# Kernel tuning notes

Hardware: AMD Instinct MI355X
Metric: run time of the kernel (lower is better)

The kernel has to match this reference:

```python
import jax, jax.numpy as jnp
import numpy as np

L, D, H, DH, DI, V, S, B = 12, 768, 12, 64, 3072, 32000, 512, 2
LN_EPS = 1e-3  # keras LayerNormalization default epsilon

def _gelu(x):
    return x * 0.5 * (1.0 + jnp.tanh(np.sqrt(2.0 / np.pi).astype(np.float32) * (x + 0.044715 * x ** 3)))

def _layer_norm(x, g, b):
    mu = jnp.mean(x, axis=-1, keepdims=True)
    var = jnp.mean((x - mu) ** 2, axis=-1, keepdims=True)
    return (x - mu) * jax.lax.rsqrt(var + LN_EPS) * g + b

def _rel_shift(x, klen):
    # x: [qlen, rlen, b, n] -> shifted [qlen, klen, b, n]
    q, r, b, n = x.shape
    x = x.reshape(r, q, b, n)[1:].reshape(q, r - 1, b, n)
    return x[:, :klen]

def _pos_emb():
    # relative positions klen..-qlen+1 (attn_type='bi', mems=None -> klen=qlen=S)
    pos_seq = jnp.arange(S, -S, -1.0, dtype=jnp.float32)                      # [2S]
    inv_freq = 1.0 / (10000.0 ** (jnp.arange(0, D, 2, dtype=jnp.float32) / D))
    sinusoid = pos_seq[:, None] * inv_freq[None, :]
    pe = jnp.concatenate([jnp.sin(sinusoid), jnp.cos(sinusoid)], axis=-1)     # [2S, D]
    return jnp.broadcast_to(pe[:, None, :], (2 * S, B, D))                    # [2S, B, D]

def setup_inputs() -> dict:
    key = jax.random.key(0)
    ks = jax.random.split(key, 12)
    rn = lambda k, sh: 0.02 * jax.random.normal(k, sh, dtype=jnp.float32)
    return {
        "inp_k": jax.random.randint(ks[0], (S, B), 0, V),
        "seg_ids": jax.random.randint(ks[1], (S, B), 0, 2),
        "input_mask": jax.random.randint(ks[2], (S, B), 0, 2),
        "lookup_table": rn(ks[3], (V, D)),
        "Wq": rn(ks[4], (L, D, H, DH)),
        "Wk": rn(ks[5], (L, D, H, DH)),
        "Wv": rn(ks[6], (L, D, H, DH)),
        "Wr": rn(ks[7], (L, D, H, DH)),
        "Wo": rn(ks[8], (L, D, H, DH)),
        "r_w_bias": rn(ks[9], (L, H, DH)),
        "r_r_bias": rn(ks[10], (L, H, DH)),
        "r_s_bias": rn(ks[11], (L, H, DH)),
        "seg_embed": rn(jax.random.fold_in(key, 100), (L, 2, H, DH)),
        "ln_attn_g": jnp.ones((L, D), jnp.float32),
        "ln_attn_b": jnp.zeros((L, D), jnp.float32),
        "ln_ff_g": jnp.ones((L, D), jnp.float32),
        "ln_ff_b": jnp.zeros((L, D), jnp.float32),
        "ff_w1": rn(jax.random.fold_in(key, 101), (L, D, DI)),
        "ff_b1": jnp.zeros((L, DI), jnp.float32),
        "ff_w2": rn(jax.random.fold_in(key, 102), (L, DI, D)),
        "ff_b2": jnp.zeros((L, D), jnp.float32),
    }

def reference(inp_k, seg_ids, input_mask, lookup_table, Wq, Wk, Wv, Wr, Wo,
              r_w_bias, r_r_bias, r_s_bias, seg_embed,
              ln_attn_g, ln_attn_b, ln_ff_g, ln_ff_b,
              ff_w1, ff_b1, ff_w2, ff_b2):
    h = lookup_table[inp_k]                                                   # [S,B,D]
    r = _pos_emb()                                                            # [2S,B,D]
    # segment "same/different" one-hot matrix [q,k,b,2]
    seg_mat = jax.nn.one_hot((seg_ids[:, None, :] != seg_ids[None, :, :]).astype(jnp.int32), 2, dtype=jnp.float32)
    attn_mask = input_mask.astype(jnp.float32)[None, :, :, None]              # [1,S,B,1] broadcast over q,heads
    scale = DH ** -0.5
    for l in range(L):
        q = jnp.einsum('ibh,hnd->ibnd', h, Wq[l])
        k = jnp.einsum('ibh,hnd->ibnd', h, Wk[l])
        v = jnp.einsum('ibh,hnd->ibnd', h, Wv[l])
        kr = jnp.einsum('ibh,hnd->ibnd', r, Wr[l])                            # [2S,B,n,d]
        ac = jnp.einsum('ibnd,jbnd->ijbn', q + r_w_bias[l], k)
        bd = _rel_shift(jnp.einsum('ibnd,jbnd->ijbn', q + r_r_bias[l], kr), S)
        ef = jnp.einsum('ibnd,snd->ibns', q + r_s_bias[l], seg_embed[l])
        ef = jnp.einsum('ijbs,ibns->ijbn', seg_mat, ef)
        score = (ac + bd + ef) * scale - 1e30 * attn_mask
        prob = jax.nn.softmax(score, axis=1)                                  # softmax over key axis j
        vec = jnp.einsum('ijbn,jbnd->ibnd', prob, v)
        h = _layer_norm(jnp.einsum('ibnd,hnd->ibh', vec, Wo[l]) + h, ln_attn_g[l], ln_attn_b[l])
        ff = _gelu(jnp.einsum('ibd,df->ibf', h, ff_w1[l]) + ff_b1[l])
        ff = jnp.einsum('ibf,fd->ibd', ff, ff_w2[l]) + ff_b2[l]
        h = _layer_norm(ff + h, ln_ff_g[l], ln_ff_b[l])
    return h
```

## Files before the change

kernel.cpp:

```cpp
#include <hip/hip_runtime.h>
#include <hip/hip_bf16.h>
#include <math.h>

#define S 512
#define B 2
#define D 768
#define H 12
#define DH 64
#define DI 3072
#define NL 12
#define NTOK (S * B)

typedef __attribute__((ext_vector_type(8))) short short8v;
typedef __attribute__((ext_vector_type(4))) float f32x4;

__device__ __forceinline__ unsigned short f2b(float f) {
  union { float f; unsigned int u; } v; v.f = f;
  unsigned int r = v.u + 0x7fffu + ((v.u >> 16) & 1u);
  return (unsigned short)(r >> 16);
}
__device__ __forceinline__ float b2f(unsigned short u) {
  union { unsigned int u; float f; } v; v.u = ((unsigned int)u) << 16;
  return v.f;
}

__device__ __forceinline__ float gelu_f(float x) {
  const float c = 0.7978845608028654f;
  float t = tanhf(c * (x + 0.044715f * x * x * x));
  return x * 0.5f * (1.0f + t);
}

__device__ __forceinline__ int vkey(int r) {
  return ((((r & 7) ^ ((r >> 3) & 7)) & 7) << 3);
}

__global__ __launch_bounds__(256) void embed_kernel(const int* __restrict__ inp_k,
                                                    const float* __restrict__ lut,
                                                    float* __restrict__ h,
                                                    unsigned short* __restrict__ h_bf) {
  int t = blockIdx.x;
  int id = inp_k[t];
  for (int j = threadIdx.x; j < D; j += 256) {
    float v = lut[(size_t)id * D + j];
    h[t * D + j] = v;
    h_bf[t * D + j] = f2b(v);
  }
}

__global__ __launch_bounds__(384) void posemb_kernel(unsigned short* __restrict__ r2b) {
  int j = blockIdx.x;
  int d = threadIdx.x;
  float pos = (float)(S - j);
  float inv_freq = expf(-logf(10000.0f) * (2.0f * (float)d / (float)D));
  float x = pos * inv_freq;
  r2b[j * D + d]       = f2b(sinf(x));
  r2b[j * D + 384 + d] = f2b(cosf(x));
}

__device__ __forceinline__ void transpose_swz(const float* __restrict__ src,
                                              unsigned short* __restrict__ dst,
                                              int K, int N, int tile, int n_base,
                                              unsigned short* __restrict__ Ls ) {
  int ntk = K >> 6;
  int tk = tile % ntk, tn = tile / ntk;
  int k0 = tk << 6, n0 = tn << 6;
  int tid = threadIdx.x;
  int kk = tid >> 4, c4 = (tid & 15) * 4;
#pragma unroll
  for (int r = 0; r < 4; ++r) {
    int k = kk + r * 16;
    float4 a = *(const float4*)&src[(size_t)(k0 + k) * N + n0 + c4];
    Ls[(c4 + 0) * 72 + k] = f2b(a.x);
    Ls[(c4 + 1) * 72 + k] = f2b(a.y);
    Ls[(c4 + 2) * 72 + k] = f2b(a.z);
    Ls[(c4 + 3) * 72 + k] = f2b(a.w);
  }
  __syncthreads();
  int nl = tid >> 2, kc0 = (tid & 3) << 4;
  int ng = n_base + n0;
  size_t tilebase = ((size_t)(ng >> 7) * ntk + tk) * 8192;
  int row = (ng & 64) + nl;
  int key = (row & 7) << 3;
  short8v v0 = *(short8v*)&Ls[nl * 72 + kc0];
  short8v v1 = *(short8v*)&Ls[nl * 72 + kc0 + 8];
  *(short8v*)&dst[tilebase + row * 64 + (kc0 ^ key)] = v0;
  *(short8v*)&dst[tilebase + row * 64 + ((kc0 + 8) ^ key)] = v1;
}

__global__ __launch_bounds__(256) void prep_all(const float* __restrict__ Wq,
                                                const float* __restrict__ Wk,
                                                const float* __restrict__ Wv,
                                                const float* __restrict__ Wr,
                                                const float* __restrict__ Wo,
                                                const float* __restrict__ W1,
                                                const float* __restrict__ W2,
                                                unsigned short* __restrict__ wqkv_t,
                                                unsigned short* __restrict__ wr_t,
                                                unsigned short* __restrict__ wo_t,
                                                unsigned short* __restrict__ w1_t,
                                                unsigned short* __restrict__ w2_t) {
  __shared__ __align__(16) unsigned short Ls[64 * 72];
  const size_t DD = (size_t)D * D;
  const size_t DDI = (size_t)D * DI;
  int tb = blockIdx.x;
  int l = tb / 1872, t2 = tb % 1872;
  int tid = threadIdx.x;
  if (t2 < 432) {
    int which = t2 / 144, tile = t2 % 144;
    const float* src = (which == 0 ? Wq : (which == 1 ? Wk : Wv)) + l * DD;
    transpose_swz(src, wqkv_t + l * 3 * DD, D, D, tile, which * D, Ls);
  } else if (t2 < 576) {
    transpose_swz(Wr + l * DD, wr_t + l * DD, D, D, t2 - 432, 0, Ls);
  } else if (t2 < 1152) {
    transpose_swz(W1 + l * DDI, w1_t + l * DDI, D, DI, t2 - 576, 0, Ls);
  } else if (t2 < 1728) {
    transpose_swz(W2 + l * DDI, w2_t + l * DDI, DI, D, t2 - 1152, 0, Ls);
  } else {
    int c = t2 - 1728;
    int tkk = c % 12, tnn = c / 12;
    int k0 = tkk << 6, n0 = tnn << 6;
    int nl = tid >> 2, kc0 = (tid & 3) << 4;
    const float* srcp = Wo + l * DD + (size_t)(n0 + nl) * D + k0 + kc0;
    float4 a0 = *(const float4*)&srcp[0];
    float4 a1 = *(const float4*)&srcp[4];
    float4 a2 = *(const float4*)&srcp[8];
    float4 a3 = *(const float4*)&srcp[12];
    short8v v0, v1;
    v0[0] = (short)f2b(a0.x); v0[1] = (short)f2b(a0.y); v0[2] = (short)f2b(a0.z); v0[3] = (short)f2b(a0.w);
    v0[4] = (short)f2b(a1.x); v0[5] = (short)f2b(a1.y); v0[6] = (short)f2b(a1.z); v0[7] = (short)f2b(a1.w);
    v1[0] = (short)f2b(a2.x); v1[1] = (short)f2b(a2.y); v1[2] = (short)f2b(a2.z); v1[3] = (short)f2b(a2.w);
    v1[4] = (short)f2b(a3.x); v1[5] = (short)f2b(a3.y); v1[6] = (short)f2b(a3.z); v1[7] = (short)f2b(a3.w);
    unsigned short* dst = wo_t + l * DD;
    size_t tilebase = ((size_t)(n0 >> 7) * 12 + tkk) * 8192;
    int row = (n0 & 64) + nl;
    int key = (row & 7) << 3;
    *(short8v*)&dst[tilebase + row * 64 + (kc0 ^ key)] = v0;
    *(short8v*)&dst[tilebase + row * 64 + ((kc0 + 8) ^ key)] = v1;
  }
}

template <int ACT, int OUTBF>
__device__ __forceinline__ void gemm_tile(const unsigned short* __restrict__ A,
                                          const unsigned short* __restrict__ Wt,
                                          const float* __restrict__ bias,
                                          float* __restrict__ Cf,
                                          unsigned short* __restrict__ Cb,
                                          int N, int K, int bm, int bn,
                                          int kbeg, int kend) {
  __shared__ __align__(16) unsigned short As[64 * 64];
  __shared__ __align__(16) unsigned short Bs[128 * 64];
  const int tid = threadIdx.x, lane = tid & 63, w = tid >> 6;
  const int l8 = lane >> 3, lm8 = lane & 7;
  const int aColByte = ((lm8 ^ l8) << 4);
  const int KT = K >> 6;
  const size_t wtn = (size_t)(bn >> 7) * KT;

  f32x4 acc[4][2];
#pragma unroll
  for (int mi = 0; mi < 4; ++mi)
#pragma unroll
    for (int ni = 0; ni < 2; ++ni)
      acc[mi][ni] = (f32x4){0.f, 0.f, 0.f, 0.f};

  for (int kt = kbeg; kt < kend; kt += 64) {
    __syncthreads();
#pragma unroll
    for (int c = 0; c < 2; ++c) {
      int row = c * 32 + w * 8 + l8;
      const char* src = (const char*)&A[(size_t)(bm + row) * K + kt] + aColByte;
      __builtin_amdgcn_global_load_lds(
          (const __attribute__((address_space(1))) void*)src,
          (__attribute__((address_space(3))) void*)((char*)As + c * 4096 + w * 1024),
          16, 0, 0);
    }
    const char* wt = (const char*)&Wt[(wtn + (kt >> 6)) * 8192];
#pragma unroll
    for (int c = 0; c < 4; ++c) {
      __builtin_amdgcn_global_load_lds(
          (const __attribute__((address_space(1))) void*)(wt + c * 4096 + w * 1024 + lane * 16),
          (__attribute__((address_space(3))) void*)((char*)Bs + c * 4096 + w * 1024),
          16, 0, 0);
    }
    __syncthreads();
#pragma unroll
    for (int ks = 0; ks < 2; ++ks) {
      const int kus = ks * 32 + (lane >> 4) * 8;
      short8v af[4], bf[2];
#pragma unroll
      for (int mi = 0; mi < 4; ++mi) {
        int row = mi * 16 + (lane & 15);
        af[mi] = *(const short8v*)&As[row * 64 + (kus ^ ((row & 7) << 3))];
      }
#pragma unroll
      for (int ni = 0; ni < 2; ++ni) {
        int row = w * 32 + ni * 16 + (lane & 15);
        bf[ni] = *(const short8v*)&Bs[row * 64 + (kus ^ ((row & 7) << 3))];
      }
#pragma unroll
      for (int mi = 0; mi < 4; ++mi)
#pragma unroll
        for (int ni = 0; ni < 2; ++ni)
          acc[mi][ni] = __builtin_amdgcn_mfma_f32_16x16x32_bf16(af[mi], bf[ni], acc[mi][ni], 0, 0, 0);
    }
  }

  int r0 = (lane >> 4) * 4, cc = lane & 15;
#pragma unroll
  for (int mi = 0; mi < 4; ++mi) {
    int row = bm + mi * 16 + r0;
#pragma unroll
    for (int ni = 0; ni < 2; ++ni) {
      int col = bn + w * 32 + ni * 16 + cc;
      float bv = bias ? bias[col] : 0.0f;
#pragma unroll
      for (int r = 0; r < 4; ++r) {
        float v = acc[mi][ni][r] + bv;
        if (ACT == 1) v = gelu_f(v);
        if (OUTBF) Cb[(size_t)(row + r) * N + col] = f2b(v);
        else       Cf[(size_t)(row + r) * N + col] = v;
      }
    }
  }
}

__global__ __launch_bounds__(256) void gemm_qkv(const unsigned short* __restrict__ h_bf,
                                                const unsigned short* __restrict__ wqkv,
                                                unsigned short* __restrict__ qkv_bf) {
  int bx = blockIdx.x;
  gemm_tile<0, 1>(h_bf, wqkv, nullptr, nullptr, qkv_bf, 2304, 768,
                  (bx / 18) * 64, (bx % 18) * 128, 0, 768);
}

__global__ __launch_bounds__(256) void gemm_kr_all(const unsigned short* __restrict__ r2_bf,
                                                   const unsigned short* __restrict__ wr_t,
                                                   unsigned short* __restrict__ kr_all) {
  int bx = blockIdx.x;
  int l = bx / 96, b2 = bx % 96;
  gemm_tile<0, 1>(r2_bf, wr_t + (size_t)l * D * D, nullptr, nullptr,
                  kr_all + (size_t)l * NTOK * D, 768, 768,
                  (b2 / 6) * 64, (b2 % 6) * 128, 0, 768);
}

template <int ACT>
__global__ __launch_bounds__(256) void gemm_bias(const unsigned short* __restrict__ A,
                                                 const unsigned short* __restrict__ W,
                                                 const float* __restrict__ bias,
                                                 unsigned short* __restrict__ C,
                                                 int N, int K, int ncb) {
  int bx = blockIdx.x;
  gemm_tile<ACT, 1>(A, W, bias, nullptr, C, N, K, (bx / ncb) * 64, (bx % ncb) * 128, 0, K);
}

__global__ __launch_bounds__(256) void gemm_splitk(const unsigned short* __restrict__ A,
                                                   const unsigned short* __restrict__ W,
                                                   float* __restrict__ part,
                                                   int N, int K, int kch) {
  int kz = blockIdx.z;
  float* Cf = part + (size_t)kz * NTOK * N;
  gemm_tile<0, 0>(A, W, nullptr, Cf, nullptr, N, K,
                  blockIdx.y * 64, blockIdx.x * 128, kz * kch, (kz + 1) * kch);
}

__global__ __launch_bounds__(256) void attn_kernel(const unsigned short* __restrict__ qkv,
                                                   const unsigned short* __restrict__ krb,
                                                   const int* __restrict__ seg_ids,
                                                   const int* __restrict__ input_mask,
                                                   const float* __restrict__ rwb,
                                                   const float* __restrict__ rrb,
                                                   const float* __restrict__ rsb,
                                                   const float* __restrict__ segemb,
                                                   unsigned short* __restrict__ vec_bf) {
  __shared__ __align__(16) char smem[51840];
  unsigned short* qw_s = (unsigned short*)(smem + 0);
  unsigned short* qr_s = (unsigned short*)(smem + 4608);
  unsigned short* k_s  = (unsigned short*)(smem + 9216);
  unsigned short* kr_s = (unsigned short*)(smem + 18432);
  unsigned short* bd_s = (unsigned short*)(smem + 32256);
  unsigned short* vt_s = (unsigned short*)(smem + 38912);
  unsigned short* pb_s = (unsigned short*)(smem + 47104);
  float* sc_s  = (float*)(smem + 9216);
  float* efs    = (float*)(smem + 51200);
  float* frow_s = (float*)(smem + 51456);
  float* rinv_s = (float*)(smem + 51584);
  int*   segrow = (int*)(smem + 51712);

  const int it = blockIdx.x * 32, b = blockIdx.y, n = blockIdx.z;
  const int tid = threadIdx.x, lane = tid & 63, w = tid >> 6;

  {
    int il = tid >> 3, d8 = (tid & 7) * 8;
    int t = (it + il) * B + b;
    short8v q0 = *(const short8v*)&qkv[(size_t)t * 2304 + n * 64 + d8];
    short8v ow0, or0;
#pragma unroll
    for (int e = 0; e < 8; ++e) {
      float f0 = b2f((unsigned short)q0[e]);
      ow0[e] = (short)f2b(f0 + rwb[n * 64 + d8 + e]);
      or0[e] = (short)f2b(f0 + rrb[n * 64 + d8 + e]);
    }
    *(short8v*)&qw_s[il * 72 + d8] = ow0;
    *(short8v*)&qr_s[il * 72 + d8] = or0;
  }
  if (tid < 64) {
    int il = tid >> 1, s = tid & 1;
    int t = (it + il) * B + b;
    float acc = 0.0f;
    for (int d = 0; d < 64; ++d)
      acc = fmaf(b2f(qkv[(size_t)t * 2304 + n * 64 + d]) + rsb[n * 64 + d],
                 segemb[(s * H + n) * 64 + d], acc);
    efs[s * 32 + il] = acc;
  }
  if (tid < 32) segrow[tid] = seg_ids[(it + tid) * B + b];

  {
#pragma unroll
    for (int c = 0; c < 2; ++c) {
      int idx = tid + c * 256;
      int row = idx >> 3, k8 = (idx & 7) * 8;
      *(short8v*)&k_s[row * 72 + k8] =
          *(const short8v*)&qkv[(size_t)(row * B + b) * 2304 + 768 + n * 64 + k8];
    }
    int u0 = 481 - it;
#pragma unroll
    for (int c = 0; c < 3; ++c) {
      int idx = tid + c * 256;
      int row = idx >> 3, k8 = (idx & 7) * 8;
      *(short8v*)&kr_s[row * 72 + k8] =
          *(const short8v*)&krb[(size_t)(u0 + row) * 768 + n * 64 + k8];
    }
  }

  f32x4 acc_v[2];
  acc_v[0] = (f32x4){0.f, 0.f, 0.f, 0.f};
  acc_v[1] = (f32x4){0.f, 0.f, 0.f, 0.f};
  float m_run = -3.0e38f;
  float rsq = 0.0f;
  const int srow = tid >> 3, sc0 = (tid & 7) * 8;

  __syncthreads();

  for (int jt = 0; jt < 512; jt += 64) {
    const int vj = tid >> 2, vd16 = (tid & 3) * 16;
    short8v vl0 = *(const short8v*)&qkv[(size_t)((jt + vj) * B + b) * 2304 + 1536 + n * 64 + vd16];
    short8v vl1 = *(const short8v*)&qkv[(size_t)((jt + vj) * B + b) * 2304 + 1536 + n * 64 + vd16 + 8];

    f32x4 jacc[3][2];
#pragma unroll
    for (int t = 0; t < 3; ++t) {
      jacc[t][0] = (f32x4){0.f, 0.f, 0.f, 0.f};
      jacc[t][1] = (f32x4){0.f, 0.f, 0.f, 0.f};
    }
#pragma unroll
    for (int ks = 0; ks < 2; ++ks) {
      int kb = ks * 32 + (lane >> 4) * 8;
      short8v aw[2], ar[2];
#pragma unroll
      for (int mi = 0; mi < 2; ++mi) {
        aw[mi] = *(const short8v*)&qw_s[(mi * 16 + (lane & 15)) * 72 + kb];
        ar[mi] = *(const short8v*)&qr_s[(mi * 16 + (lane & 15)) * 72 + kb];
      }
      {
        short8v bk = *(const short8v*)&k_s[(w * 16 + (lane & 15)) * 72 + kb];
        jacc[0][0] = __builtin_amdgcn_mfma_f32_16x16x32_bf16(aw[0], bk, jacc[0][0], 0, 0, 0);
        jacc[0][1] = __builtin_amdgcn_mfma_f32_16x16x32_bf16(aw[1], bk, jacc[0][1], 0, 0, 0);
      }
      {
        short8v br = *(const short8v*)&kr_s[(w * 16 + (lane & 15)) * 72 + kb];
        jacc[1][0] = __builtin_amdgcn_mfma_f32_16x16x32_bf16(ar[0], br, jacc[1][0], 0, 0, 0);
        jacc[1][1] = __builtin_amdgcn_mfma_f32_16x16x32_bf16(ar[1], br, jacc[1][1], 0, 0, 0);
      }
      if (w < 2) {
        short8v br = *(const short8v*)&kr_s[((w + 4) * 16 + (lane & 15)) * 72 + kb];
        jacc[2][0] = __builtin_amdgcn_mfma_f32_16x16x32_bf16(ar[0], br, jacc[2][0], 0, 0, 0);
        jacc[2][1] = __builtin_amdgcn_mfma_f32_16x16x32_bf16(ar[1], br, jacc[2][1], 0, 0, 0);
      }
    }
#pragma unroll
    for (int t = 1; t < 3; ++t) {
      int cf = w + (t - 1) * 4;
      if (t == 1 || w < 2) {
#pragma unroll
        for (int mi = 0; mi < 2; ++mi)
#pragma unroll
          for (int r = 0; r < 4; ++r)
            bd_s[(mi * 16 + (lane >> 4) * 4 + r) * 104 + cf * 16 + (lane & 15)] =
                f2b(jacc[t][mi][r]);
      }
    }
    __syncthreads();

    {
      int jl = w * 16 + (lane & 15);
      int jg = jt + jl;
      float maskterm = -1e30f * (float)input_mask[jg * B + b];
      int segj = seg_ids[jg * B + b];
#pragma unroll
      for (int mi = 0; mi < 2; ++mi)
#pragma unroll
        for (int r = 0; r < 4; ++r) {
          int il = mi * 16 + (lane >> 4) * 4 + r;
          float bd = b2f(bd_s[il * 104 + 31 - il + jl]);
          float e = efs[(segrow[il] != segj ? 1 : 0) * 32 + il];
          sc_s[il * 68 + jl] = (jacc[0][mi][r] + bd + e) * 0.125f + maskterm;
        }
    }
    __syncthreads();

    {
      float4 f0 = *(const float4*)&sc_s[srow * 68 + sc0];
      float4 f1 = *(const float4*)&sc_s[srow * 68 + sc0 + 4];
      float mx = fmaxf(fmaxf(fmaxf(f0.x, f0.y), fmaxf(f0.z, f0.w)),
                       fmaxf(fmaxf(f1.x, f1.y), fmaxf(f1.z, f1.w)));
      mx = fmaxf(mx, __shfl_xor(mx, 1, 8));
      mx = fmaxf(mx, __shfl_xor(mx, 2, 8));
      mx = fmaxf(mx, __shfl_xor(mx, 4, 8));
      float mnew = fmaxf(m_run, mx);
      float fsc = __expf(m_run - mnew);
      m_run = mnew;
      float p0 = __expf(f0.x - mnew), p1 = __expf(f0.y - mnew);
      float p2 = __expf(f0.z - mnew), p3 = __expf(f0.w - mnew);
      float p4 = __expf(f1.x - mnew), p5 = __expf(f1.y - mnew);
      float p6 = __expf(f1.z - mnew), p7 = __expf(f1.w - mnew);
      rsq = rsq * fsc + ((p0 + p1 + p2 + p3) + (p4 + p5 + p6 + p7));
      short8v o0;
      o0[0] = (short)f2b(p0); o0[1] = (short)f2b(p1); o0[2] = (short)f2b(p2); o0[3] = (short)f2b(p3);
      o0[4] = (short)f2b(p4); o0[5] = (short)f2b(p5); o0[6] = (short)f2b(p6); o0[7] = (short)f2b(p7);
      *(short8v*)&pb_s[srow * 64 + (sc0 ^ vkey(srow))] = o0;
      if ((tid & 7) == 0) frow_s[srow] = fsc;
#pragma unroll
      for (int e = 0; e < 8; ++e) {
        int d0 = vd16 + e, d1 = vd16 + 8 + e;
        vt_s[d0 * 64 + (vj ^ vkey(d0))] = (unsigned short)vl0[e];
        vt_s[d1 * 64 + (vj ^ vkey(d1))] = (unsigned short)vl1[e];
      }
    }
    __syncthreads();

#pragma unroll
    for (int mi = 0; mi < 2; ++mi) {
#pragma unroll
      for (int r = 0; r < 4; ++r)
        acc_v[mi][r] *= frow_s[mi * 16 + (lane >> 4) * 4 + r];
    }
#pragma unroll
    for (int ks = 0; ks < 2; ++ks) {
      int kb = ks * 32 + (lane >> 4) * 8;
      int vrow = w * 16 + (lane & 15);
      short8v bv = *(const short8v*)&vt_s[vrow * 64 + (kb ^ vkey(vrow))];
#pragma unroll
      for (int mi = 0; mi < 2; ++mi) {
        int prow = mi * 16 + (lane & 15);
        short8v ap = *(const short8v*)&pb_s[prow * 64 + (kb ^ vkey(prow))];
        acc_v[mi] = __builtin_amdgcn_mfma_f32_16x16x32_bf16(ap, bv, acc_v[mi], 0, 0, 0);
      }
    }
    if (jt < 448) {
      int jn = jt + 64;
#pragma unroll
      for (int c = 0; c < 2; ++c) {
        int idx = tid + c * 256;
        int row = idx >> 3, k8 = (idx & 7) * 8;
        *(short8v*)&k_s[row * 72 + k8] =
            *(const short8v*)&qkv[(size_t)((jn + row) * B + b) * 2304 + 768 + n * 64 + k8];
      }
      int u0 = 481 - it + jn;
#pragma unroll
      for (int c = 0; c < 3; ++c) {
        int idx = tid + c * 256;
        int row = idx >> 3, k8 = (idx & 7) * 8;
        *(short8v*)&kr_s[row * 72 + k8] =
            *(const short8v*)&krb[(size_t)(u0 + row) * 768 + n * 64 + k8];
      }
    }
    __syncthreads();
  }

  {
    float tot = rsq;
    tot += __shfl_xor(tot, 1, 8);
    tot += __shfl_xor(tot, 2, 8);
    tot += __shfl_xor(tot, 4, 8);
    if ((tid & 7) == 0) rinv_s[srow] = 1.0f / tot;
  }
  __syncthreads();

#pragma unroll
  for (int mi = 0; mi < 2; ++mi)
#pragma unroll
    for (int r = 0; r < 4; ++r) {
      int row = mi * 16 + (lane >> 4) * 4 + r;
      int d = w * 16 + (lane & 15);
      int t = (it + row) * B + b;
      vec_bf[(size_t)t * D + n * 64 + d] = f2b(acc_v[mi][r] * rinv_s[row]);
    }
}

template <int P, int HASBIAS>
__global__ __launch_bounds__(256) void add_ln_reduce(const float* __restrict__ part,
                                                     const float* __restrict__ bias,
                                                     float* __restrict__ h,
                                                     unsigned short* __restrict__ h_bf,
                                                     const float* __restrict__ g,
                                                     const float* __restrict__ bi) {
  int t = blockIdx.x;
  int tid = threadIdx.x;
  __shared__ float red[256];
  float vx = 0.f, vy = 0.f, vz = 0.f, vw = 0.f;
  float s = 0.0f;
  int c = tid * 4;
  if (tid < 192) {
    float4 x = {0.f, 0.f, 0.f, 0.f};
#pragma unroll
    for (int p = 0; p < P; ++p) {
      float4 pp = *(const float4*)&part[(size_t)p * NTOK * D + (size_t)t * D + c];
      x.x += pp.x; x.y += pp.y; x.z += pp.z; x.w += pp.w;
    }
    if (HASBIAS) {
      float4 bb = *(const float4*)&bias[c];
      x.x += bb.x; x.y += bb.y; x.z += bb.z; x.w += bb.w;
    }
    float4 hh = *(const float4*)&h[(size_t)t * D + c];
    vx = x.x + hh.x; vy = x.y + hh.y; vz = x.z + hh.z; vw = x.w + hh.w;
    s = vx + vy + vz + vw;
  }
  red[tid] = s;
  __syncthreads();
  for (int st = 128; st > 0; st >>= 1) {
    if (tid < st) red[tid] += red[tid + st];
    __syncthreads();
  }
  float mu = red[0] / (float)D;
  __syncthreads();
  float s2 = 0.0f;
  if (tid < 192) {
    float dx = vx - mu, dy = vy - mu, dz = vz - mu, dw = vw - mu;
    s2 = dx * dx + dy * dy + dz * dz + dw * dw;
  }
  red[tid] = s2;
  __syncthreads();
  for (int st = 128; st > 0; st >>= 1) {
    if (tid < st) red[tid] += red[tid + st];
    __syncthreads();
  }
  float var = red[0] / (float)D;
  float rstd = rsqrtf(var + 1e-3f);
  __syncthreads();
  if (tid < 192) {
    float4 gg = *(const float4*)&g[c];
    float4 bb = *(const float4*)&bi[c];
    float o0 = (vx - mu) * rstd * gg.x + bb.x;
    float o1 = (vy - mu) * rstd * gg.y + bb.y;
    float o2 = (vz - mu) * rstd * gg.z + bb.z;
    float o3 = (vw - mu) * rstd * gg.w + bb.w;
    float4 of = {o0, o1, o2, o3};
    *(float4*)&h[(size_t)t * D + c] = of;
    ushort4 ob;
    ob.x = f2b(o0); ob.y = f2b(o1); ob.z = f2b(o2); ob.w = f2b(o3);
    *(ushort4*)&h_bf[(size_t)t * D + c] = ob;
  }
}

extern "C" void kernel_launch(void* const* d_in, const int* in_sizes, int n_in,
                              void* d_out, int out_size, void* d_ws, size_t ws_size,
                              hipStream_t stream) {
  const int*   inp_k      = (const int*)d_in[0];
  const int*   seg_ids    = (const int*)d_in[1];
  const int*   input_mask = (const int*)d_in[2];
  const float* lut        = (const float*)d_in[3];
  const float* Wq         = (const float*)d_in[4];
  const float* Wk         = (const float*)d_in[5];
  const float* Wv         = (const float*)d_in[6];
  const float* Wr         = (const float*)d_in[7];
  const float* Wo         = (const float*)d_in[8];
  const float* r_w_bias   = (const float*)d_in[9];
  const float* r_r_bias   = (const float*)d_in[10];
  const float* r_s_bias   = (const float*)d_in[11];
  const float* seg_embed  = (const float*)d_in[12];
  const float* ln_attn_g  = (const float*)d_in[13];
  const float* ln_attn_b  = (const float*)d_in[14];
  const float* ln_ff_g    = (const float*)d_in[15];
  const float* ln_ff_b    = (const float*)d_in[16];
  const float* ff_w1      = (const float*)d_in[17];
  const float* ff_b1      = (const float*)d_in[18];
  const float* ff_w2      = (const float*)d_in[19];
  const float* ff_b2      = (const float*)d_in[20];

  float* h = (float*)d_out;
  char* wp = (char*)d_ws;
  auto alloc = [&](size_t bytes) -> void* {
    void* p = (void*)wp;
    wp += (bytes + 255) & ~(size_t)255;
    return p;
  };
  const size_t TOKD = (size_t)NTOK * D;
  const size_t DD = (size_t)D * D;
  const size_t DDI = (size_t)D * DI;
  unsigned short* qkv_bf = (unsigned short*)alloc((size_t)NTOK * 2304 * 2);
  unsigned short* kr_all = (unsigned short*)alloc((size_t)NL * TOKD * 2);
  unsigned short* h_bf   = (unsigned short*)alloc(TOKD * 2);
  unsigned short* r2_bf  = (unsigned short*)alloc(TOKD * 2);
  unsigned short* vec_bf = (unsigned short*)alloc(TOKD * 2);
  unsigned short* ff1_bf = (unsigned short*)alloc((size_t)NTOK * DI * 2);
  float* part = (float*)alloc((size_t)4 * TOKD * 4);
  unsigned short* wqkv_t = (unsigned short*)alloc((size_t)NL * 3 * DD * 2);
  unsigned short* wr_t   = (unsigned short*)alloc((size_t)NL * DD * 2);
  unsigned short* wo_t   = (unsigned short*)alloc((size_t)NL * DD * 2);
  unsigned short* w1_t   = (unsigned short*)alloc((size_t)NL * DDI * 2);
  unsigned short* w2_t   = (unsigned short*)alloc((size_t)NL * DDI * 2);

  prep_all<<<NL * 1872, 256, 0, stream>>>(Wq, Wk, Wv, Wr, Wo, ff_w1, ff_w2,
                                          wqkv_t, wr_t, wo_t, w1_t, w2_t);
  embed_kernel<<<NTOK, 256, 0, stream>>>(inp_k, lut, h, h_bf);
  posemb_kernel<<<2 * S, 384, 0, stream>>>(r2_bf);
  gemm_kr_all<<<NL * 96, 256, 0, stream>>>(r2_bf, wr_t, kr_all);

  for (int l = 0; l < NL; ++l) {
    gemm_qkv<<<288, 256, 0, stream>>>(h_bf, wqkv_t + (size_t)l * 3 * DD, qkv_bf);

    attn_kernel<<<dim3(16, B, H), 256, 0, stream>>>(
        qkv_bf, kr_all + (size_t)l * TOKD, seg_ids, input_mask,
        r_w_bias + (size_t)l * D, r_r_bias + (size_t)l * D,
        r_s_bias + (size_t)l * D, seg_embed + (size_t)l * 2 * H * DH,
        vec_bf);

    gemm_splitk<<<dim3(6, 16, 2), 256, 0, stream>>>(
        vec_bf, wo_t + (size_t)l * DD, part, D, D, 384);
    add_ln_reduce<2, 0><<<NTOK, 256, 0, stream>>>(
        part, nullptr, h, h_bf, ln_attn_g + (size_t)l * D, ln_attn_b + (size_t)l * D);

    gemm_bias<1><<<24 * 16, 256, 0, stream>>>(
        h_bf, w1_t + (size_t)l * DDI, ff_b1 + (size_t)l * DI, ff1_bf, DI, D, 24);

    gemm_splitk<<<dim3(6, 16, 4), 256, 0, stream>>>(
        ff1_bf, w2_t + (size_t)l * DDI, part, D, DI, 768);
    add_ln_reduce<4, 1><<<NTOK, 256, 0, stream>>>(
        part, ff_b2 + (size_t)l * D, h, h_bf, ln_ff_g + (size_t)l * D, ln_ff_b + (size_t)l * D);
  }
}
```

Measured before the change: 1.300 ms.

## Fuse split-K reduction and residual LayerNorm into GEMM via last-block counter

Merges the split-K partial-sum reduction, bias add, residual add and LayerNorm into the split-K GEMM kernel. Each block increments a per-row-tile atomic counter, and the last block to finish a 64-row tile performs the reduction and normalization with wave-level shuffles. This removes two kernel launches per layer and the separate reduction pass, at the cost of a serialized tail done by one block per row tile with fewer threads than the old per-token LN kernel.

```diff
diff --git a/kernel.cpp b/kernel.cpp
--- a/kernel.cpp
+++ b/kernel.cpp
@@ -251,14 +251,102 @@
   gemm_tile<ACT, 1>(A, W, bias, nullptr, C, N, K, (bx / ncb) * 64, (bx % ncb) * 128, 0, K);
 }
 
-__global__ __launch_bounds__(256) void gemm_splitk(const unsigned short* __restrict__ A,
-                                                   const unsigned short* __restrict__ W,
-                                                   float* __restrict__ part,
-                                                   int N, int K, int kch) {
+template <int P>
+__device__ __forceinline__ float4 sum_part(const float* __restrict__ part, int t, int c) {
+  float4 a = *(const float4*)&part[(size_t)t * D + c];
+#pragma unroll
+  for (int p = 1; p < P; ++p) {
+    float4 b = *(const float4*)&part[(size_t)p * NTOK * D + (size_t)t * D + c];
+    a.x += b.x; a.y += b.y; a.z += b.z; a.w += b.w;
+  }
+  return a;
+}
+
+template <int P, int HASBIAS>
+__global__ __launch_bounds__(256) void gemm_splitk_ln(const unsigned short* __restrict__ A,
+                                                      const unsigned short* __restrict__ Wt,
+                                                      float* __restrict__ part,
+                                                      const float* __restrict__ bias,
+                                                      float* __restrict__ h,
+                                                      unsigned short* __restrict__ h_bf,
+                                                      const float* __restrict__ g,
+                                                      const float* __restrict__ bi,
+                                                      int* __restrict__ counters,
+                                                      int K, int kch) {
   int kz = blockIdx.z;
-  float* Cf = part + (size_t)kz * NTOK * N;
-  gemm_tile<0, 0>(A, W, nullptr, Cf, nullptr, N, K,
+  float* Cf = part + (size_t)kz * NTOK * D;
+  gemm_tile<0, 0>(A, Wt, nullptr, Cf, nullptr, D, K,
                   blockIdx.y * 64, blockIdx.x * 128, kz * kch, (kz + 1) * kch);
+
+  __shared__ int slast;
+  const int tid = threadIdx.x;
+  __threadfence();
+  __syncthreads();
+  if (tid == 0) {
+    int done = __hip_atomic_fetch_add(&counters[blockIdx.y], 1, __ATOMIC_ACQ_REL,
+                                      __HIP_MEMORY_SCOPE_AGENT);
+    slast = (done == 6 * P - 1) ? 1 : 0;
+    if (slast)
+      __hip_atomic_store(&counters[blockIdx.y], 0, __ATOMIC_RELAXED,
+                         __HIP_MEMORY_SCOPE_AGENT);
+  }
+  __syncthreads();
+  if (!slast) return;
+  __threadfence();
+
+  const int wv = tid >> 6, lane = tid & 63;
+  const int c0 = lane * 4;
+#pragma unroll 2
+  for (int i = 0; i < 16; ++i) {
+    const int t = blockIdx.y * 64 + wv * 16 + i;
+    float4 v0 = sum_part<P>(part, t, c0);
+    float4 v1 = sum_part<P>(part, t, c0 + 256);
+    float4 v2 = sum_part<P>(part, t, c0 + 512);
+    if (HASBIAS) {
+      float4 b0 = *(const float4*)&bias[c0];
+      float4 b1 = *(const float4*)&bias[c0 + 256];
+      float4 b2 = *(const float4*)&bias[c0 + 512];
+      v0.x += b0.x; v0.y += b0.y; v0.z += b0.z; v0.w += b0.w;
+      v1.x += b1.x; v1.y += b1.y; v1.z += b1.z; v1.w += b1.w;
+      v2.x += b2.x; v2.y += b2.y; v2.z += b2.z; v2.w += b2.w;
+    }
+    float4 h0 = *(const float4*)&h[(size_t)t * D + c0];
+    float4 h1 = *(const float4*)&h[(size_t)t * D + c0 + 256];
+    float4 h2 = *(const float4*)&h[(size_t)t * D + c0 + 512];
+    v0.x += h0.x; v0.y += h0.y; v0.z += h0.z; v0.w += h0.w;
+    v1.x += h1.x; v1.y += h1.y; v1.z += h1.z; v1.w += h1.w;
+    v2.x += h2.x; v2.y += h2.y; v2.z += h2.z; v2.w += h2.w;
+    float s = (v0.x + v0.y + v0.z + v0.w) + (v1.x + v1.y + v1.z + v1.w) +
+              (v2.x + v2.y + v2.z + v2.w);
+#pragma unroll
+    for (int m = 1; m < 64; m <<= 1) s += __shfl_xor(s, m, 64);
+    float mu = s * (1.0f / (float)D);
+    float d0x = v0.x - mu, d0y = v0.y - mu, d0z = v0.z - mu, d0w = v0.w - mu;
+    float d1x = v1.x - mu, d1y = v1.y - mu, d1z = v1.z - mu, d1w = v1.w - mu;
+    float d2x = v2.x - mu, d2y = v2.y - mu, d2z = v2.z - mu, d2w = v2.w - mu;
+    float s2 = d0x * d0x + d0y * d0y + d0z * d0z + d0w * d0w +
+               d1x * d1x + d1y * d1y + d1z * d1z + d1w * d1w +
+               d2x * d2x + d2y * d2y + d2z * d2z + d2w * d2w;
+#pragma unroll
+    for (int m = 1; m < 64; m <<= 1) s2 += __shfl_xor(s2, m, 64);
+    float rstd = rsqrtf(s2 * (1.0f / (float)D) + 1e-3f);
+#pragma unroll
+    for (int j = 0; j < 3; ++j) {
+      int c = c0 + j * 256;
+      float4 vv = (j == 0) ? v0 : (j == 1 ? v1 : v2);
+      float4 gg = *(const float4*)&g[c];
+      float4 bb = *(const float4*)&bi[c];
+      float o0 = (vv.x - mu) * rstd * gg.x + bb.x;
+      float o1 = (vv.y - mu) * rstd * gg.y + bb.y;
+      float o2 = (vv.z - mu) * rstd * gg.z + bb.z;
+      float o3 = (vv.w - mu) * rstd * gg.w + bb.w;
+      float4 of = {o0, o1, o2, o3};
+      *(float4*)&h[(size_t)t * D + c] = of;
+      ushort4 ob;
+      ob.x = f2b(o0); ob.y = f2b(o1); ob.z = f2b(o2); ob.w = f2b(o3);
+      *(ushort4*)&h_bf[(size_t)t * D + c] = ob;
+    }
+  }
 }
 
 __global__ __launch_bounds__(256) void attn_kernel(const unsigned short* __restrict__ qkv,
@@ -493,71 +581,6 @@
       int t = (it + row) * B + b;
       vec_bf[(size_t)t * D + n * 64 + d] = f2b(acc_v[mi][r] * rinv_s[row]);
     }
-}
-
-template <int P, int HASBIAS>
-__global__ __launch_bounds__(256) void add_ln_reduce(const float* __restrict__ part,
-                                                     const float* __restrict__ bias,
-                                                     float* __restrict__ h,
-                                                     unsigned short* __restrict__ h_bf,
-                                                     const float* __restrict__ g,
-                                                     const float* __restrict__ bi) {
-  int t = blockIdx.x;
-  int tid = threadIdx.x;
-  __shared__ float red[256];
-  float vx = 0.f, vy = 0.f, vz = 0.f, vw = 0.f;
-  float s = 0.0f;
-  int c = tid * 4;
-  if (tid < 192) {
-    float4 x = {0.f, 0.f, 0.f, 0.f};
-#pragma unroll
-    for (int p = 0; p < P; ++p) {
-      float4 pp = *(const float4*)&part[(size_t)p * NTOK * D + (size_t)t * D + c];
-      x.x += pp.x; x.y += pp.y; x.z += pp.z; x.w += pp.w;
-    }
-    if (HASBIAS) {
-      float4 bb = *(const float4*)&bias[c];
-      x.x += bb.x; x.y += bb.y; x.z += bb.z; x.w += bb.w;
-    }
-    float4 hh = *(const float4*)&h[(size_t)t * D + c];
-    vx = x.x + hh.x; vy = x.y + hh.y; vz = x.z + hh.z; vw = x.w + hh.w;
-    s = vx + vy + vz + vw;
-  }
-  red[tid] = s;
-  __syncthreads();
-  for (int st = 128; st > 0; st >>= 1) {
-    if (tid < st) red[tid] += red[tid + st];
-    __syncthreads();
-  }
-  float mu = red[0] / (float)D;
-  __syncthreads();
-  float s2 = 0.0f;
-  if (tid < 192) {
-    float dx = vx - mu, dy = vy - mu, dz = vz - mu, dw = vw - mu;
-    s2 = dx * dx + dy * dy + dz * dz + dw * dw;
-  }
-  red[tid] = s2;
-  __syncthreads();
-  for (int st = 128; st > 0; st >>= 1) {
-    if (tid < st) red[tid] += red[tid + st];
-    __syncthreads();
-  }
-  float var = red[0] / (float)D;
-  float rstd = rsqrtf(var + 1e-3f);
-  __syncthreads();
-  if (tid < 192) {
-    float4 gg = *(const float4*)&g[c];
-    float4 bb = *(const float4*)&bi[c];
-    float o0 = (vx - mu) * rstd * gg.x + bb.x;
-    float o1 = (vy - mu) * rstd * gg.y + bb.y;
-    float o2 = (vz - mu) * rstd * gg.z + bb.z;
-    float o3 = (vw - mu) * rstd * gg.w + bb.w;
-    float4 of = {o0, o1, o2, o3};
-    *(float4*)&h[(size_t)t * D + c] = of;
-    ushort4 ob;
-    ob.x = f2b(o0); ob.y = f2b(o1); ob.z = f2b(o2); ob.w = f2b(o3);
-    *(ushort4*)&h_bf[(size_t)t * D + c] = ob;
-  }
 }
 
 extern "C" void kernel_launch(void* const* d_in, const int* in_sizes, int n_in,
@@ -602,12 +625,14 @@
   unsigned short* vec_bf = (unsigned short*)alloc(TOKD * 2);
   unsigned short* ff1_bf = (unsigned short*)alloc((size_t)NTOK * DI * 2);
   float* part = (float*)alloc((size_t)4 * TOKD * 4);
+  int* counters = (int*)alloc(64 * 4);
   unsigned short* wqkv_t = (unsigned short*)alloc((size_t)NL * 3 * DD * 2);
   unsigned short* wr_t   = (unsigned short*)alloc((size_t)NL * DD * 2);
   unsigned short* wo_t   = (unsigned short*)alloc((size_t)NL * DD * 2);
   unsigned short* w1_t   = (unsigned short*)alloc((size_t)NL * DDI * 2);
   unsigned short* w2_t   = (unsigned short*)alloc((size_t)NL * DDI * 2);
 
+  (void)hipMemsetAsync(counters, 0, 64 * 4, stream);
   prep_all<<<NL * 1872, 256, 0, stream>>>(Wq, Wk, Wv, Wr, Wo, ff_w1, ff_w2,
                                           wqkv_t, wr_t, wo_t, w1_t, w2_t);
   embed_kernel<<<NTOK, 256, 0, stream>>>(inp_k, lut, h, h_bf);
@@ -623,17 +648,15 @@
         r_s_bias + (size_t)l * D, seg_embed + (size_t)l * 2 * H * DH,
         vec_bf);
 
-    gemm_splitk<<<dim3(6, 16, 2), 256, 0, stream>>>(
-        vec_bf, wo_t + (size_t)l * DD, part, D, D, 384);
-    add_ln_reduce<2, 0><<<NTOK, 256, 0, stream>>>(
-        part, nullptr, h, h_bf, ln_attn_g + (size_t)l * D, ln_attn_b + (size_t)l * D);
+    gemm_splitk_ln<2, 0><<<dim3(6, 16, 2), 256, 0, stream>>>(
+        vec_bf, wo_t + (size_t)l * DD, part, nullptr, h, h_bf,
+        ln_attn_g + (size_t)l * D, ln_attn_b + (size_t)l * D, counters, D, 384);
 
     gemm_bias<1><<<24 * 16, 256, 0, stream>>>(
         h_bf, w1_t + (size_t)l * DDI, ff_b1 + (size_t)l * DI, ff1_bf, DI, D, 24);
 
-    gemm_splitk<<<dim3(6, 16, 4), 256, 0, stream>>>(
-        ff1_bf, w2_t + (size_t)l * DDI, part, D, DI, 768);
-    add_ln_reduce<4, 1><<<NTOK, 256, 0, stream>>>(
-        part, ff_b2 + (size_t)l * D, h, h_bf, ln_ff_g + (size_t)l * D, ln_ff_b + (size_t)l * D);
-  }
-}
+    gemm_splitk_ln<4, 1><<<dim3(6, 16, 4), 256, 0, stream>>>(
+        ff1_bf, w2_t + (size_t)l * DDI, part, ff_b2 + (size_t)l * D, h, h_bf,
+        ln_ff_g + (size_t)l * D, ln_ff_b + (size_t)l * D, counters, DI, 768);
+  }
+}
```

New measurement: 2.618 ms. +101.4%, slower.
